# Kernel tuning notes

Hardware: AMD Instinct MI355X
Metric: run time of the kernel (lower is better)

Reference implementation:

```python
import jax, jax.numpy as jnp
import numpy as np

H = 2048
B, L, S = 4, 4096, 10

def setup_inputs() -> dict:
    key = jax.random.key(0)
    k1, k2, k3, k4, k5, k6 = jax.random.split(key, 6)
    scale = 1.0 / np.sqrt(H)
    return {
        "h_english": jax.random.normal(k1, (B, L, H), dtype=jnp.float32),
        "h_lojban": jax.random.normal(k2, (B, S, H), dtype=jnp.float32),
        "w_q": jax.random.normal(k3, (H, H), dtype=jnp.float32) * scale,
        "w_k": jax.random.normal(k4, (H, H), dtype=jnp.float32) * scale,
        "w_v": jax.random.normal(k5, (H, H), dtype=jnp.float32) * scale,
        "w_o": jax.random.normal(k6, (H, H), dtype=jnp.float32) * scale,
        "alpha": jnp.float32(0.1),
    }

def reference(h_english, h_lojban, w_q, w_k, w_v, w_o, alpha):
    h = h_english.shape[-1]
    # torch Linear: y = x @ W^T
    q = jnp.einsum('blh,oh->blo', h_english, w_q)   # [B,L,H]
    k = jnp.einsum('bsh,oh->bso', h_lojban, w_k)    # [B,S,H]
    v = jnp.einsum('bsh,oh->bso', h_lojban, w_v)    # [B,S,H]
    scores = jnp.einsum('blh,bsh->bls', q, k) / jnp.sqrt(jnp.float32(h))  # [B,L,S]
    probs = jax.nn.softmax(scores, axis=-1)
    context = jnp.einsum('bls,bsh->blh', probs, v)  # [B,L,H]
    delta = jnp.einsum('blh,oh->blo', context, w_o)
    return h_english + alpha * delta
```

## Files before the change

kernel.cpp:

```cpp
#include <hip/hip_runtime.h>

#define SDIM 10
#define HDIM 2048
#define LDIM 4096

#define KSCALE 0.02209708691207961f

__global__ __launch_bounds__(256) void kv_kernel(
    const float* __restrict__ h_l, const float* __restrict__ w_k,
    const float* __restrict__ w_v, float* __restrict__ k_out,
    float* __restrict__ v_out) {
  const int b = blockIdx.y;
  const int wave = threadIdx.x >> 6;
  const int lane = threadIdx.x & 63;
  const int o_sub = lane & 7;
  const int hsplit = lane >> 3;
  const int o = blockIdx.x * 32 + wave * 8 + o_sub;

  const float4* hl4 = (const float4*)(h_l + (size_t)b * SDIM * HDIM) + hsplit * 64;
  const float4* wk4 = (const float4*)(w_k + (size_t)o * HDIM) + hsplit * 64;
  const float4* wv4 = (const float4*)(w_v + (size_t)o * HDIM) + hsplit * 64;

  float acck[SDIM], accv[SDIM];
#pragma unroll
  for (int s = 0; s < SDIM; s++) { acck[s] = 0.f; accv[s] = 0.f; }

  for (int i = 0; i < 64; i++) {
    float4 wk = wk4[i];
    float4 wv = wv4[i];
#pragma unroll
    for (int s = 0; s < SDIM; s++) {
      float4 hv = hl4[(size_t)s * 512 + i];
      acck[s] += wk.x * hv.x + wk.y * hv.y + wk.z * hv.z + wk.w * hv.w;
      accv[s] += wv.x * hv.x + wv.y * hv.y + wv.z * hv.z + wv.w * hv.w;
    }
  }
#pragma unroll
  for (int s = 0; s < SDIM; s++) {
    acck[s] += __shfl_xor(acck[s], 8);
    acck[s] += __shfl_xor(acck[s], 16);
    acck[s] += __shfl_xor(acck[s], 32);
    accv[s] += __shfl_xor(accv[s], 8);
    accv[s] += __shfl_xor(accv[s], 16);
    accv[s] += __shfl_xor(accv[s], 32);
  }
  if (hsplit == 0) {
#pragma unroll
    for (int s = 0; s < SDIM; s++) {
      k_out[((size_t)b * SDIM + s) * HDIM + o] = acck[s];
      v_out[((size_t)b * SDIM + s) * HDIM + o] = accv[s];
    }
  }
}

__global__ __launch_bounds__(256) void kk_kernel(
    const float* __restrict__ k_in, const float* __restrict__ w_q,
    float* __restrict__ kk_out) {
  const int b = blockIdx.y;
  const int wave = threadIdx.x >> 6;
  const int lane = threadIdx.x & 63;
  const int h_sub = lane & 15;
  const int osplit = lane >> 4;
  const int h = blockIdx.x * 64 + wave * 16 + h_sub;
  const float* kb = k_in + (size_t)b * SDIM * HDIM;

  float acc[SDIM];
#pragma unroll
  for (int s = 0; s < SDIM; s++) acc[s] = 0.f;

  const int o0 = osplit * 512;
  for (int o4 = 0; o4 < 128; o4++) {
    const int o = o0 + o4 * 4;
    float w0 = w_q[(size_t)(o + 0) * HDIM + h];
    float w1 = w_q[(size_t)(o + 1) * HDIM + h];
    float w2 = w_q[(size_t)(o + 2) * HDIM + h];
    float w3 = w_q[(size_t)(o + 3) * HDIM + h];
#pragma unroll
    for (int s = 0; s < SDIM; s++) {
      const float4 kv = *(const float4*)(kb + (size_t)s * HDIM + o);
      acc[s] += kv.x * w0 + kv.y * w1 + kv.z * w2 + kv.w * w3;
    }
  }
#pragma unroll
  for (int s = 0; s < SDIM; s++) {
    acc[s] += __shfl_xor(acc[s], 16);
    acc[s] += __shfl_xor(acc[s], 32);
  }
  if (osplit == 0) {
#pragma unroll
    for (int s = 0; s < SDIM; s++)
      kk_out[((size_t)b * SDIM + s) * HDIM + h] = acc[s];
  }
}

__global__ __launch_bounds__(256) void vo_kernel(
    const float* __restrict__ v_in, const float* __restrict__ w_o,
    float* __restrict__ vo_out) {
  const int b = blockIdx.y;
  const int wave = threadIdx.x >> 6;
  const int lane = threadIdx.x & 63;
  const int o_sub = lane & 7;
  const int hsplit = lane >> 3;
  const int o = blockIdx.x * 32 + wave * 8 + o_sub;

  const float4* vb4 = (const float4*)(v_in + (size_t)b * SDIM * HDIM) + hsplit * 64;
  const float4* wo4 = (const float4*)(w_o + (size_t)o * HDIM) + hsplit * 64;

  float acc[SDIM];
#pragma unroll
  for (int s = 0; s < SDIM; s++) acc[s] = 0.f;

  for (int i = 0; i < 64; i++) {
    float4 wv = wo4[i];
#pragma unroll
    for (int s = 0; s < SDIM; s++) {
      float4 hv = vb4[(size_t)s * 512 + i];
      acc[s] += wv.x * hv.x + wv.y * hv.y + wv.z * hv.z + wv.w * hv.w;
    }
  }
#pragma unroll
  for (int s = 0; s < SDIM; s++) {
    acc[s] += __shfl_xor(acc[s], 8);
    acc[s] += __shfl_xor(acc[s], 16);
    acc[s] += __shfl_xor(acc[s], 32);
  }
  if (hsplit == 0) {
#pragma unroll
    for (int s = 0; s < SDIM; s++)
      vo_out[((size_t)b * SDIM + s) * HDIM + o] = acc[s];
  }
}

__global__ __launch_bounds__(256, 2) void attn_kernel(
    const float* __restrict__ h_e, const float* __restrict__ kk,
    const float* __restrict__ vo, const float* __restrict__ alpha_p,
    float* __restrict__ out) {
  const int b = blockIdx.y;
  const int wave = threadIdx.x >> 6;
  const int lane = threadIdx.x & 63;
  const int row0 = blockIdx.x * 16 + wave * 4;
  const float alpha = *alpha_p;
  const float* kkb = kk + (size_t)b * SDIM * HDIM;
  const float* vob = vo + (size_t)b * SDIM * HDIM;
  const size_t rowbase = ((size_t)b * LDIM + row0) * HDIM;

  float4 he[4][8];
#pragma unroll
  for (int r = 0; r < 4; r++) {
    const float4* src = (const float4*)(h_e + rowbase + (size_t)r * HDIM);
#pragma unroll
    for (int i = 0; i < 8; i++) he[r][i] = src[i * 64 + lane];
  }

  float acc[4][SDIM];
#pragma unroll
  for (int r = 0; r < 4; r++)
#pragma unroll
    for (int s = 0; s < SDIM; s++) acc[r][s] = 0.f;

#pragma unroll
  for (int i = 0; i < 8; i++) {
#pragma unroll
    for (int s = 0; s < SDIM; s++) {
      float4 kv = ((const float4*)(kkb + (size_t)s * HDIM))[i * 64 + lane];
#pragma unroll
      for (int r = 0; r < 4; r++)
        acc[r][s] += he[r][i].x * kv.x + he[r][i].y * kv.y +
                     he[r][i].z * kv.z + he[r][i].w * kv.w;
    }
  }

#pragma unroll
  for (int r = 0; r < 4; r++)
#pragma unroll
    for (int s = 0; s < SDIM; s++) {
      float v = acc[r][s];
      v += __shfl_xor(v, 1);
      v += __shfl_xor(v, 2);
      v += __shfl_xor(v, 4);
      v += __shfl_xor(v, 8);
      v += __shfl_xor(v, 16);
      v += __shfl_xor(v, 32);
      acc[r][s] = v * KSCALE;
    }

#pragma unroll
  for (int r = 0; r < 4; r++) {
    float m = acc[r][0];
#pragma unroll
    for (int s = 1; s < SDIM; s++) m = fmaxf(m, acc[r][s]);
    float sum = 0.f;
#pragma unroll
    for (int s = 0; s < SDIM; s++) {
      acc[r][s] = __expf(acc[r][s] - m);
      sum += acc[r][s];
    }
    const float inv = alpha / sum;
#pragma unroll
    for (int s = 0; s < SDIM; s++) acc[r][s] *= inv;
  }

#pragma unroll
  for (int i = 0; i < 8; i++) {
    float4 o4[4];
#pragma unroll
    for (int r = 0; r < 4; r++) o4[r] = he[r][i];
#pragma unroll
    for (int s = 0; s < SDIM; s++) {
      float4 vv = ((const float4*)(vob + (size_t)s * HDIM))[i * 64 + lane];
#pragma unroll
      for (int r = 0; r < 4; r++) {
        o4[r].x += acc[r][s] * vv.x;
        o4[r].y += acc[r][s] * vv.y;
        o4[r].z += acc[r][s] * vv.z;
        o4[r].w += acc[r][s] * vv.w;
      }
    }
#pragma unroll
    for (int r = 0; r < 4; r++)
      ((float4*)(out + rowbase + (size_t)r * HDIM))[i * 64 + lane] = o4[r];
  }
}

extern "C" void kernel_launch(void* const* d_in, const int* in_sizes, int n_in,
                              void* d_out, int out_size, void* d_ws, size_t ws_size,
                              hipStream_t stream) {
  const float* h_e   = (const float*)d_in[0];
  const float* h_l   = (const float*)d_in[1];
  const float* w_q   = (const float*)d_in[2];
  const float* w_k   = (const float*)d_in[3];
  const float* w_v   = (const float*)d_in[4];
  const float* w_o   = (const float*)d_in[5];
  const float* alpha = (const float*)d_in[6];
  float* out = (float*)d_out;

  float* ws    = (float*)d_ws;
  float* k_ws  = ws;
  float* v_ws  = ws + 81920;
  float* kk_ws = ws + 163840;
  float* vo_ws = ws + 245760;

  kv_kernel<<<dim3(64, 4), 256, 0, stream>>>(h_l, w_k, w_v, k_ws, v_ws);
  kk_kernel<<<dim3(32, 4), 256, 0, stream>>>(k_ws, w_q, kk_ws);
  vo_kernel<<<dim3(64, 4), 256, 0, stream>>>(v_ws, w_o, vo_ws);
  attn_kernel<<<dim3(256, 4), 256, 0, stream>>>(h_e, kk_ws, vo_ws, alpha, out);
}
```

Measured before the change: 482.8 us.

## Restructure small projection kernels for more parallelism and split-K kk reduction

Each wave in the kv and vo kernels now computes two output rows and spreads the full H dimension across its lanes with fully coalesced float4 loads, and the grid grows to four times as many blocks. The kk kernel, which read w_q columns with strided loads, becomes a split-K kernel: k is staged in shared memory, w_q rows are read coalesced, and partial sums go to a workspace that a separate reduce kernel adds up. The attention kernel handles two rows per wave instead of four and drops the occupancy hint, to lower register pressure and add blocks. This adds one kernel launch, a partial-sum buffer in workspace and longer shuffle reductions.

```diff
diff --git a/kernel.cpp b/kernel.cpp
--- a/kernel.cpp
+++ b/kernel.cpp
@@ -3,6 +3,7 @@
 #define SDIM 10
 #define HDIM 2048
 #define LDIM 4096
+#define BDIM 4
 
 #define KSCALE 0.02209708691207961f
 
@@ -13,84 +14,102 @@
   const int b = blockIdx.y;
   const int wave = threadIdx.x >> 6;
   const int lane = threadIdx.x & 63;
-  const int o_sub = lane & 7;
-  const int hsplit = lane >> 3;
-  const int o = blockIdx.x * 32 + wave * 8 + o_sub;
-
-  const float4* hl4 = (const float4*)(h_l + (size_t)b * SDIM * HDIM) + hsplit * 64;
-  const float4* wk4 = (const float4*)(w_k + (size_t)o * HDIM) + hsplit * 64;
-  const float4* wv4 = (const float4*)(w_v + (size_t)o * HDIM) + hsplit * 64;
-
-  float acck[SDIM], accv[SDIM];
-#pragma unroll
-  for (int s = 0; s < SDIM; s++) { acck[s] = 0.f; accv[s] = 0.f; }
-
-  for (int i = 0; i < 64; i++) {
-    float4 wk = wk4[i];
-    float4 wv = wv4[i];
-#pragma unroll
-    for (int s = 0; s < SDIM; s++) {
-      float4 hv = hl4[(size_t)s * 512 + i];
-      acck[s] += wk.x * hv.x + wk.y * hv.y + wk.z * hv.z + wk.w * hv.w;
-      accv[s] += wv.x * hv.x + wv.y * hv.y + wv.z * hv.z + wv.w * hv.w;
+  const int opair = blockIdx.x * 4 + wave;
+  const int o0 = opair * 2;
+
+  const float4* hl4 = (const float4*)(h_l + (size_t)b * SDIM * HDIM);
+  const float4* wk0 = (const float4*)(w_k + (size_t)o0 * HDIM);
+  const float4* wk1 = (const float4*)(w_k + (size_t)(o0 + 1) * HDIM);
+  const float4* wv0 = (const float4*)(w_v + (size_t)o0 * HDIM);
+  const float4* wv1 = (const float4*)(w_v + (size_t)(o0 + 1) * HDIM);
+
+  float ak0[SDIM], ak1[SDIM], av0[SDIM], av1[SDIM];
+#pragma unroll
+  for (int s = 0; s < SDIM; s++) { ak0[s] = ak1[s] = av0[s] = av1[s] = 0.f; }
+
+#pragma unroll
+  for (int j = 0; j < 8; j++) {
+    const int idx = j * 64 + lane;
+    const float4 a0 = wk0[idx], a1 = wk1[idx];
+    const float4 c0 = wv0[idx], c1 = wv1[idx];
+#pragma unroll
+    for (int s = 0; s < SDIM; s++) {
+      const float4 h = hl4[s * 512 + idx];
+      ak0[s] += a0.x * h.x + a0.y * h.y + a0.z * h.z + a0.w * h.w;
+      ak1[s] += a1.x * h.x + a1.y * h.y + a1.z * h.z + a1.w * h.w;
+      av0[s] += c0.x * h.x + c0.y * h.y + c0.z * h.z + c0.w * h.w;
+      av1[s] += c1.x * h.x + c1.y * h.y + c1.z * h.z + c1.w * h.w;
     }
   }
 #pragma unroll
   for (int s = 0; s < SDIM; s++) {
-    acck[s] += __shfl_xor(acck[s], 8);
-    acck[s] += __shfl_xor(acck[s], 16);
-    acck[s] += __shfl_xor(acck[s], 32);
-    accv[s] += __shfl_xor(accv[s], 8);
-    accv[s] += __shfl_xor(accv[s], 16);
-    accv[s] += __shfl_xor(accv[s], 32);
-  }
-  if (hsplit == 0) {
-#pragma unroll
-    for (int s = 0; s < SDIM; s++) {
-      k_out[((size_t)b * SDIM + s) * HDIM + o] = acck[s];
-      v_out[((size_t)b * SDIM + s) * HDIM + o] = accv[s];
-    }
-  }
-}
-
-__global__ __launch_bounds__(256) void kk_kernel(
+#pragma unroll
+    for (int d = 1; d < 64; d <<= 1) {
+      ak0[s] += __shfl_xor(ak0[s], d);
+      ak1[s] += __shfl_xor(ak1[s], d);
+      av0[s] += __shfl_xor(av0[s], d);
+      av1[s] += __shfl_xor(av1[s], d);
+    }
+  }
+  if (lane == 0) {
+#pragma unroll
+    for (int s = 0; s < SDIM; s++) {
+      const size_t base = ((size_t)b * SDIM + s) * HDIM + o0;
+      k_out[base]     = ak0[s];
+      k_out[base + 1] = ak1[s];
+      v_out[base]     = av0[s];
+      v_out[base + 1] = av1[s];
+    }
+  }
+}
+
+#define OSPLIT 16
+__global__ __launch_bounds__(256) void kk_part_kernel(
     const float* __restrict__ k_in, const float* __restrict__ w_q,
-    float* __restrict__ kk_out) {
-  const int b = blockIdx.y;
-  const int wave = threadIdx.x >> 6;
-  const int lane = threadIdx.x & 63;
-  const int h_sub = lane & 15;
-  const int osplit = lane >> 4;
-  const int h = blockIdx.x * 64 + wave * 16 + h_sub;
-  const float* kb = k_in + (size_t)b * SDIM * HDIM;
-
-  float acc[SDIM];
-#pragma unroll
-  for (int s = 0; s < SDIM; s++) acc[s] = 0.f;
-
-  const int o0 = osplit * 512;
-  for (int o4 = 0; o4 < 128; o4++) {
-    const int o = o0 + o4 * 4;
-    float w0 = w_q[(size_t)(o + 0) * HDIM + h];
-    float w1 = w_q[(size_t)(o + 1) * HDIM + h];
-    float w2 = w_q[(size_t)(o + 2) * HDIM + h];
-    float w3 = w_q[(size_t)(o + 3) * HDIM + h];
-#pragma unroll
-    for (int s = 0; s < SDIM; s++) {
-      const float4 kv = *(const float4*)(kb + (size_t)s * HDIM + o);
-      acc[s] += kv.x * w0 + kv.y * w1 + kv.z * w2 + kv.w * w3;
-    }
-  }
-#pragma unroll
-  for (int s = 0; s < SDIM; s++) {
-    acc[s] += __shfl_xor(acc[s], 16);
-    acc[s] += __shfl_xor(acc[s], 32);
-  }
-  if (osplit == 0) {
-#pragma unroll
-    for (int s = 0; s < SDIM; s++)
-      kk_out[((size_t)b * SDIM + s) * HDIM + h] = acc[s];
-  }
+    float* __restrict__ part) {
+  const int b = blockIdx.z;
+  const int oc = blockIdx.y >> 1;
+  const int s0 = (blockIdx.y & 1) * 5;
+  const int f4 = blockIdx.x * 256 + threadIdx.x;
+
+  __shared__ float ksh[5 * 128];
+  for (int idx = threadIdx.x; idx < 5 * 128; idx += 256) {
+    const int s = idx >> 7, oo = idx & 127;
+    ksh[idx] = k_in[((size_t)b * SDIM + s0 + s) * HDIM + oc * 128 + oo];
+  }
+  __syncthreads();
+
+  float4 acc[5];
+#pragma unroll
+  for (int s = 0; s < 5; s++) acc[s] = make_float4(0.f, 0.f, 0.f, 0.f);
+
+  const float4* wq4 = (const float4*)w_q;
+  for (int oo = 0; oo < 128; oo++) {
+    const float4 w = wq4[(size_t)(oc * 128 + oo) * 512 + f4];
+#pragma unroll
+    for (int s = 0; s < 5; s++) {
+      const float kv = ksh[s * 128 + oo];
+      acc[s].x += kv * w.x; acc[s].y += kv * w.y;
+      acc[s].z += kv * w.z; acc[s].w += kv * w.w;
+    }
+  }
+#pragma unroll
+  for (int s = 0; s < 5; s++) {
+    ((float4*)part)[(((size_t)oc * BDIM + b) * SDIM + s0 + s) * 512 + f4] = acc[s];
+  }
+}
+
+__global__ __launch_bounds__(256) void kk_reduce_kernel(
+    const float* __restrict__ part, float* __restrict__ kk_out) {
+  const int t = blockIdx.x * 256 + threadIdx.x;
+  const float4* p4 = (const float4*)part;
+  float4 acc = make_float4(0.f, 0.f, 0.f, 0.f);
+#pragma unroll
+  for (int p = 0; p < OSPLIT; p++) {
+    const float4 v = p4[(size_t)p * 20480 + t];
+    acc.x += v.x; acc.y += v.y; acc.z += v.z; acc.w += v.w;
+  }
+  ((float4*)kk_out)[t] = acc;
 }
 
 __global__ __launch_bounds__(256) void vo_kernel(
@@ -99,62 +118,70 @@
   const int b = blockIdx.y;
   const int wave = threadIdx.x >> 6;
   const int lane = threadIdx.x & 63;
-  const int o_sub = lane & 7;
-  const int hsplit = lane >> 3;
-  const int o = blockIdx.x * 32 + wave * 8 + o_sub;
-
-  const float4* vb4 = (const float4*)(v_in + (size_t)b * SDIM * HDIM) + hsplit * 64;
-  const float4* wo4 = (const float4*)(w_o + (size_t)o * HDIM) + hsplit * 64;
-
-  float acc[SDIM];
-#pragma unroll
-  for (int s = 0; s < SDIM; s++) acc[s] = 0.f;
-
-  for (int i = 0; i < 64; i++) {
-    float4 wv = wo4[i];
-#pragma unroll
-    for (int s = 0; s < SDIM; s++) {
-      float4 hv = vb4[(size_t)s * 512 + i];
-      acc[s] += wv.x * hv.x + wv.y * hv.y + wv.z * hv.z + wv.w * hv.w;
+  const int opair = blockIdx.x * 4 + wave;
+  const int o0 = opair * 2;
+
+  const float4* vb4 = (const float4*)(v_in + (size_t)b * SDIM * HDIM);
+  const float4* wo0 = (const float4*)(w_o + (size_t)o0 * HDIM);
+  const float4* wo1 = (const float4*)(w_o + (size_t)(o0 + 1) * HDIM);
+
+  float a0[SDIM], a1[SDIM];
+#pragma unroll
+  for (int s = 0; s < SDIM; s++) { a0[s] = a1[s] = 0.f; }
+
+#pragma unroll
+  for (int j = 0; j < 8; j++) {
+    const int idx = j * 64 + lane;
+    const float4 w0 = wo0[idx], w1 = wo1[idx];
+#pragma unroll
+    for (int s = 0; s < SDIM; s++) {
+      const float4 h = vb4[s * 512 + idx];
+      a0[s] += w0.x * h.x + w0.y * h.y + w0.z * h.z + w0.w * h.w;
+      a1[s] += w1.x * h.x + w1.y * h.y + w1.z * h.z + w1.w * h.w;
     }
   }
 #pragma unroll
   for (int s = 0; s < SDIM; s++) {
-    acc[s] += __shfl_xor(acc[s], 8);
-    acc[s] += __shfl_xor(acc[s], 16);
-    acc[s] += __shfl_xor(acc[s], 32);
-  }
-  if (hsplit == 0) {
-#pragma unroll
-    for (int s = 0; s < SDIM; s++)
-      vo_out[((size_t)b * SDIM + s) * HDIM + o] = acc[s];
-  }
-}
-
-__global__ __launch_bounds__(256, 2) void attn_kernel(
+#pragma unroll
+    for (int d = 1; d < 64; d <<= 1) {
+      a0[s] += __shfl_xor(a0[s], d);
+      a1[s] += __shfl_xor(a1[s], d);
+    }
+  }
+  if (lane == 0) {
+#pragma unroll
+    for (int s = 0; s < SDIM; s++) {
+      const size_t base = ((size_t)b * SDIM + s) * HDIM + o0;
+      vo_out[base]     = a0[s];
+      vo_out[base + 1] = a1[s];
+    }
+  }
+}
+
+__global__ __launch_bounds__(256) void attn_kernel(
     const float* __restrict__ h_e, const float* __restrict__ kk,
     const float* __restrict__ vo, const float* __restrict__ alpha_p,
     float* __restrict__ out) {
   const int b = blockIdx.y;
   const int wave = threadIdx.x >> 6;
   const int lane = threadIdx.x & 63;
-  const int row0 = blockIdx.x * 16 + wave * 4;
+  const int row0 = blockIdx.x * 8 + wave * 2;
   const float alpha = *alpha_p;
-  const float* kkb = kk + (size_t)b * SDIM * HDIM;
-  const float* vob = vo + (size_t)b * SDIM * HDIM;
+  const float4* kkb = (const float4*)(kk + (size_t)b * SDIM * HDIM);
+  const float4* vob = (const float4*)(vo + (size_t)b * SDIM * HDIM);
   const size_t rowbase = ((size_t)b * LDIM + row0) * HDIM;
 
-  float4 he[4][8];
-#pragma unroll
-  for (int r = 0; r < 4; r++) {
+  float4 he[2][8];
+#pragma unroll
+  for (int r = 0; r < 2; r++) {
     const float4* src = (const float4*)(h_e + rowbase + (size_t)r * HDIM);
 #pragma unroll
     for (int i = 0; i < 8; i++) he[r][i] = src[i * 64 + lane];
   }
 
-  float acc[4][SDIM];
-#pragma unroll
-  for (int r = 0; r < 4; r++)
+  float acc[2][SDIM];
+#pragma unroll
+  for (int r = 0; r < 2; r++)
 #pragma unroll
     for (int s = 0; s < SDIM; s++) acc[r][s] = 0.f;
 
@@ -162,16 +189,16 @@
   for (int i = 0; i < 8; i++) {
 #pragma unroll
     for (int s = 0; s < SDIM; s++) {
-      float4 kv = ((const float4*)(kkb + (size_t)s * HDIM))[i * 64 + lane];
-#pragma unroll
-      for (int r = 0; r < 4; r++)
+      const float4 kv = kkb[s * 512 + i * 64 + lane];
+#pragma unroll
+      for (int r = 0; r < 2; r++)
         acc[r][s] += he[r][i].x * kv.x + he[r][i].y * kv.y +
                      he[r][i].z * kv.z + he[r][i].w * kv.w;
     }
   }
 
 #pragma unroll
-  for (int r = 0; r < 4; r++)
+  for (int r = 0; r < 2; r++)
 #pragma unroll
     for (int s = 0; s < SDIM; s++) {
       float v = acc[r][s];
@@ -185,7 +212,7 @@
     }
 
 #pragma unroll
-  for (int r = 0; r < 4; r++) {
+  for (int r = 0; r < 2; r++) {
     float m = acc[r][0];
 #pragma unroll
     for (int s = 1; s < SDIM; s++) m = fmaxf(m, acc[r][s]);
@@ -202,14 +229,14 @@
 
 #pragma unroll
   for (int i = 0; i < 8; i++) {
-    float4 o4[4];
-#pragma unroll
-    for (int r = 0; r < 4; r++) o4[r] = he[r][i];
-#pragma unroll
-    for (int s = 0; s < SDIM; s++) {
-      float4 vv = ((const float4*)(vob + (size_t)s * HDIM))[i * 64 + lane];
-#pragma unroll
-      for (int r = 0; r < 4; r++) {
+    float4 o4[2];
+#pragma unroll
+    for (int r = 0; r < 2; r++) o4[r] = he[r][i];
+#pragma unroll
+    for (int s = 0; s < SDIM; s++) {
+      const float4 vv = vob[s * 512 + i * 64 + lane];
+#pragma unroll
+      for (int r = 0; r < 2; r++) {
         o4[r].x += acc[r][s] * vv.x;
         o4[r].y += acc[r][s] * vv.y;
         o4[r].z += acc[r][s] * vv.z;
@@ -217,7 +244,7 @@
       }
     }
 #pragma unroll
-    for (int r = 0; r < 4; r++)
+    for (int r = 0; r < 2; r++)
       ((float4*)(out + rowbase + (size_t)r * HDIM))[i * 64 + lane] = o4[r];
   }
 }
@@ -234,14 +261,16 @@
   const float* alpha = (const float*)d_in[6];
   float* out = (float*)d_out;
 
-  float* ws    = (float*)d_ws;
-  float* k_ws  = ws;
-  float* v_ws  = ws + 81920;
-  float* kk_ws = ws + 163840;
-  float* vo_ws = ws + 245760;
-
-  kv_kernel<<<dim3(64, 4), 256, 0, stream>>>(h_l, w_k, w_v, k_ws, v_ws);
-  kk_kernel<<<dim3(32, 4), 256, 0, stream>>>(k_ws, w_q, kk_ws);
-  vo_kernel<<<dim3(64, 4), 256, 0, stream>>>(v_ws, w_o, vo_ws);
-  attn_kernel<<<dim3(256, 4), 256, 0, stream>>>(h_e, kk_ws, vo_ws, alpha, out);
-}
+  float* ws      = (float*)d_ws;
+  float* k_ws    = ws;
+  float* v_ws    = ws + 81920;
+  float* kk_ws   = ws + 163840;
+  float* vo_ws   = ws + 245760;
+  float* part_ws = ws + 327680;
+
+  kv_kernel<<<dim3(256, BDIM), 256, 0, stream>>>(h_l, w_k, w_v, k_ws, v_ws);
+  kk_part_kernel<<<dim3(2, 32, BDIM), 256, 0, stream>>>(k_ws, w_q, part_ws);
+  vo_kernel<<<dim3(256, BDIM), 256, 0, stream>>>(v_ws, w_o, vo_ws);
+  kk_reduce_kernel<<<80, 256, 0, stream>>>(part_ws, kk_ws);
+  attn_kernel<<<dim3(512, BDIM), 256, 0, stream>>>(h_e, kk_ws, vo_ws, alpha, out);
+}
```

Result: faster. 412.1 us (-14.6%).
